# Performance work log

Hardware: AMD Instinct MI355X
Metric: run time of the kernel (lower is better)

The kernel has to match this reference:

```python
import jax, jax.numpy as jnp
import numpy as np
from jax import lax

B, A, T, D, V, K = 16, 1024, 512, 256, 50000, 3
EXP_DILS = [1, 2, 4, 8, 16, 32, 32]  # conv_num=7, exp_num=5
REF_DILS = [1, 1, 1]                 # refine_num=3


def setup_inputs() -> dict:
    key = jax.random.key(0)
    ks = jax.random.split(key, 14)
    inp = {
        'article_word': jax.random.randint(ks[0], (B, A), 0, V),
        'article_char': jax.random.randint(ks[1], (B, A, 16), 0, 100),
        'template_word': jax.random.randint(ks[2], (B, T), 0, V),
        'template_char': jax.random.randint(ks[3], (B, T, 16), 0, 100),
        'article_mask': jnp.ones((B, A), jnp.float32),
        'template_mask': jnp.ones((B, T), jnp.float32),
        'emb': jax.random.normal(ks[4], (V, D), jnp.float32) * 0.02,
        'exp_w': jax.random.normal(ks[5], (7, K, D, 2 * D), jnp.float32) * 0.03,
        'exp_b': jnp.zeros((7, 2 * D), jnp.float32),
        'ref_w': jax.random.normal(ks[6], (3, K, D, 2 * D), jnp.float32) * 0.03,
        'ref_b': jnp.zeros((3, 2 * D), jnp.float32),
        'ff1_w': jax.random.normal(ks[7], (10, 10), jnp.float32) * 0.3,
        'ff1_b': jnp.zeros((10,), jnp.float32),
        'ff2_w': jax.random.normal(ks[8], (10, 1), jnp.float32) * 0.3,
        'ff2_b': jnp.zeros((1,), jnp.float32),
    }
    return inp


def _res_block(x, w, b, dilation):
    # x: [B, L, D]; w: [K, D, 2D]  (Conv1d, padding='same' given k//2*dilation)
    pad = (K // 2) * dilation
    y = lax.conv_general_dilated(x, w, window_strides=(1,), padding=[(pad, pad)],
                                 rhs_dilation=(dilation,),
                                 dimension_numbers=('NWC', 'WIO', 'NWC')) + b
    a, g = jnp.split(y, 2, axis=2)  # GLU on channel dim
    return x + a * jax.nn.sigmoid(g)


def _encode(x, exp_w, exp_b, ref_w, ref_b):
    for i, d in enumerate(EXP_DILS):
        x = _res_block(x, exp_w[i], exp_b[i], d)
    for i, d in enumerate(REF_DILS):
        x = _res_block(x, ref_w[i], ref_b[i], d)
    return x  # dropout is identity in eval mode


def reference(article_word, article_char, template_word, template_char,
              article_mask, template_mask, emb, exp_w, exp_b, ref_w, ref_b,
              ff1_w, ff1_b, ff2_w, ff2_b):
    art = _encode(emb[article_word], exp_w, exp_b, ref_w, ref_b)    # [B,A,D]
    tpl = _encode(emb[template_word], exp_w, exp_b, ref_w, ref_b)   # [B,T,D]
    # pairwise squared distance without materializing [B,A,T,D]
    a2 = jnp.sum(art * art, axis=-1)                 # [B,A]
    t2 = jnp.sum(tpl * tpl, axis=-1)                 # [B,T]
    dot = jnp.einsum('bad,btd->bat', art, tpl)       # [B,A,T]
    dist = jnp.maximum(a2[:, :, None] + t2[:, None, :] - 2.0 * dot, 0.0)
    S = jnp.exp(-dist) * article_mask[:, :, None] * template_mask[:, None, :]
    row_max = jnp.max(S, axis=2)                     # [B,A]
    top, _ = lax.top_k(row_max, 10)                  # sorted descending, [B,10]
    h = jax.nn.relu(top @ ff1_w + ff1_b)             # [B,10]
    out = (h @ ff2_w + ff2_b).squeeze()              # [B]
    return out
```

## Files before the change

### kernel.cpp

```cpp
#include <hip/hip_runtime.h>
#include <math.h>

#define NB 16
#define NA 1024
#define NT 512
#define ND 256
#define PAD 32

typedef short bf8_t __attribute__((ext_vector_type(8)));
typedef float f4_t __attribute__((ext_vector_type(4)));

__device__ __forceinline__ float bf2f(ushort u) {
    union { unsigned int i; float f; } v; v.i = ((unsigned int)u) << 16; return v.f;
}
__device__ __forceinline__ ushort f2bf(float f) {
    union { float f; unsigned int i; } v; v.f = f;
    unsigned int x = v.i;
    unsigned int r = (x + 0x7fffu + ((x >> 16) & 1u)) >> 16;
    return (ushort)r;
}
__device__ __forceinline__ void gl_lds16(const void* g, void* l) {
    __builtin_amdgcn_global_load_lds(
        (const __attribute__((address_space(1))) unsigned int*)g,
        (__attribute__((address_space(3))) unsigned int*)l, 16, 0, 0);
}


__global__ void pad_zero(ushort* __restrict__ art_a, ushort* __restrict__ art_b,
                         ushort* __restrict__ tpl_a, ushort* __restrict__ tpl_b) {
    int y = blockIdx.y;
    ushort* p = (y == 0) ? art_a : (y == 1) ? art_b : (y == 2) ? tpl_a : tpl_b;
    int L = (y < 2) ? NA : NT;
    int Lp = L + 2 * PAD;
    int idx = blockIdx.x * 256 + threadIdx.x;
    int plane = idx >> 6;
    int row_in = idx & 63;
    int slab = (row_in < PAD) ? row_in : L + row_in;
    uint4 z = make_uint4(0, 0, 0, 0);
    *(uint4*)(p + ((size_t)plane * Lp + slab) * 8) = z;
}

__global__ void gather_emb_bf16(const int* __restrict__ words,
                                const float* __restrict__ emb,
                                ushort* __restrict__ out, int Lbits, int Lp, int n) {
    int idx = blockIdx.x * 256 + threadIdx.x;
    if (idx >= n) return;
    int L = 1 << Lbits;
    int l = idx & (L - 1);
    int bq = idx >> Lbits;
    int qq = bq & 31, b = bq >> 5;
    int wd = words[b * L + l];
    const float4* src = (const float4*)(emb + (size_t)wd * ND + qq * 8);
    float4 v0 = src[0], v1 = src[1];
    ushort o[8];
    o[0]=f2bf(v0.x); o[1]=f2bf(v0.y); o[2]=f2bf(v0.z); o[3]=f2bf(v0.w);
    o[4]=f2bf(v1.x); o[5]=f2bf(v1.y); o[6]=f2bf(v1.z); o[7]=f2bf(v1.w);
    *(uint4*)(out + ((size_t)bq * Lp + PAD + l) * 8) = *(uint4*)o;
}

__global__ void __launch_bounds__(256)
repack_w(const float* __restrict__ exp_w, const float* __restrict__ ref_w,
         ushort* __restrict__ wpack) {
    __shared__ float tile[64][65];
    int li = blockIdx.z;
    int gk = blockIdx.x;
    int gc = blockIdx.y;
    const float* src = (li < 7) ? exp_w + (size_t)li * 3 * ND * 512
                                : ref_w + (size_t)(li - 7) * 3 * ND * 512;
    int k0g = gk * 64, c0 = gc * 64;
    int tid = threadIdx.x;
    #pragma unroll
    for (int p = 0; p < 4; ++p) {
        int kr = p * 16 + (tid >> 4);
        int cc = (tid & 15) * 4;
        *(float4*)&tile[kr][cc] =
            *(const float4*)(src + (size_t)(k0g + kr) * 512 + c0 + cc);
    }
    __syncthreads();
    int tap = k0g >> 8, kl0 = k0g & 255, kc0 = kl0 >> 5;
    int ag = c0 >> 8, cb = (c0 & 255) >> 6;
    int kg = tid >> 5, idx = tid & 31;
    int kc = kc0 + (kg >> 2), qq = kg & 3;
    #pragma unroll
    for (int h = 0; h < 2; ++h) {
        int w64 = idx + h * 32;
        int cprime = h * 64 + ag * 32 + idx;
        ushort o[8];
        #pragma unroll
        for (int j = 0; j < 8; ++j) o[j] = f2bf(tile[kg * 8 + j][w64]);
        ushort* d = wpack +
            (((((size_t)(li * 4 + cb) * 3 + tap) * 8 + kc) * 4 + qq) * 128 + cprime) * 8;
        *(uint4*)d = *(uint4*)o;
    }
}

__global__ void __launch_bounds__(256, 3)
conv_glu_mfma(const ushort* __restrict__ art_x, ushort* __restrict__ art_y,
              const ushort* __restrict__ tpl_x, ushort* __restrict__ tpl_y,
              const ushort* __restrict__ wp, const float* __restrict__ bias,
              int dil) {
    __shared__ char smem[34816];
    ushort* Als = (ushort*)smem;
    float* ylds = (float*)smem;

    const int tid = threadIdx.x;
    const int w = tid >> 6, lane = tid & 63;
    const int wm = w >> 1, wn = w & 1;
    const int q = lane >> 4, l15 = lane & 15;

    const int b = blockIdx.z;
    const int plane = blockIdx.y;
    const int cb = blockIdx.x;
    const int b32 = b * 32;

    int Lp, l0;
    const ushort* xb;
    ushort* yb;
    if (plane < 8) {
        Lp = NA + 2 * PAD; l0 = plane * 128;
        xb = art_x; yb = art_y;
    } else {
        Lp = NT + 2 * PAD; l0 = (plane - 8) * 128;
        xb = tpl_x; yb = tpl_y;
    }
    const ushort* wl = wp + (size_t)cb * 98304;
    const int boff = (q * 128 + wn * 64 + l15) * 8;

    f4_t acc[4][4];
    #pragma unroll
    for (int i = 0; i < 4; ++i)
        #pragma unroll
        for (int j = 0; j < 4; ++j)
            acc[i][j] = (f4_t){0.f, 0.f, 0.f, 0.f};

    for (int kc = 0; kc < 8; ++kc) {
        bf8_t bfr[3][4];
        const ushort* wkc = wl + kc * 4096 + boff;
        #pragma unroll
        for (int t = 0; t < 3; ++t)
            #pragma unroll
            for (int nt = 0; nt < 4; ++nt)
                bfr[t][nt] = *(const bf8_t*)(wkc + t * 32768 + nt * 128);

        #pragma unroll
        for (int s3 = 0; s3 < 3; ++s3) {
            int s = w + s3 * 4;
            int qq = kc * 4 + s / 3;
            int rphys = l0 + (s % 3) * 64 + lane;
            gl_lds16(xb + ((size_t)(b32 + qq) * Lp + rphys) * 8, Als + s * 512);
        }
        __syncthreads();

        #pragma unroll
        for (int t = 0; t < 3; ++t) {
            const int sh = (t - 1) * dil;
            bf8_t af[4];
            #pragma unroll
            for (int mt = 0; mt < 4; ++mt)
                af[mt] = *(const bf8_t*)(Als + (q * 192 + 32 + sh + wm * 64 + mt * 16 + l15) * 8);
            #pragma unroll
            for (int mt = 0; mt < 4; ++mt)
                #pragma unroll
                for (int nt = 0; nt < 4; ++nt)
                    acc[mt][nt] = __builtin_amdgcn_mfma_f32_16x16x32_bf16(
                        af[mt], bfr[t][nt], acc[mt][nt], 0, 0, 0);
        }
        __syncthreads();
    }

    #pragma unroll
    for (int nt = 0; nt < 2; ++nt) {
        const int cl = wn * 32 + nt * 16 + l15;
        const int chan = cb * 64 + cl;
        const float ba = bias[chan];
        const float bg2 = bias[chan + 256];
        #pragma unroll
        for (int mt = 0; mt < 4; ++mt) {
            #pragma unroll
            for (int r = 0; r < 4; ++r) {
                const int row = wm * 64 + mt * 16 + q * 4 + r;
                float av = acc[mt][nt][r] + ba;
                float gv = acc[mt][nt + 2][r] + bg2;
                ylds[row * 68 + cl] = av / (1.f + __expf(-gv));
            }
        }
    }
    __syncthreads();

    #pragma unroll
    for (int p = 0; p < 4; ++p) {
        int u = p * 256 + tid;
        int cl8 = u >> 7;
        int row = u & 127;
        size_t go = ((size_t)(b32 + cb * 8 + cl8) * Lp + l0 + PAD + row) * 8;
        ushort xv[8]; *(uint4*)xv = *(const uint4*)(xb + go);
        float4 y0 = *(float4*)&ylds[row * 68 + cl8 * 8];
        float4 y1 = *(float4*)&ylds[row * 68 + cl8 * 8 + 4];
        ushort ov[8];
        ov[0]=f2bf(bf2f(xv[0])+y0.x); ov[1]=f2bf(bf2f(xv[1])+y0.y);
        ov[2]=f2bf(bf2f(xv[2])+y0.z); ov[3]=f2bf(bf2f(xv[3])+y0.w);
        ov[4]=f2bf(bf2f(xv[4])+y1.x); ov[5]=f2bf(bf2f(xv[5])+y1.y);
        ov[6]=f2bf(bf2f(xv[6])+y1.z); ov[7]=f2bf(bf2f(xv[7])+y1.w);
        *(uint4*)(yb + go) = *(uint4*)ov;
    }
}

__global__ void sumsq_bf16(const ushort* __restrict__ x, float* __restrict__ out,
                           int L, int Lp) {
    __shared__ float red[4][64];
    int tid = threadIdx.x;
    int r = tid & 63, pg = tid >> 6;
    int row_g = blockIdx.x * 64 + r;
    int b = row_g / L, l = row_g - b * L;
    float s = 0.f;
    #pragma unroll
    for (int j = 0; j < 8; ++j) {
        int qq = pg * 8 + j;
        const ushort* p = x + ((size_t)(b * 32 + qq) * Lp + PAD + l) * 8;
        ushort v[8]; *(uint4*)v = *(const uint4*)p;
        #pragma unroll
        for (int e = 0; e < 8; ++e) { float f = bf2f(v[e]); s += f * f; }
    }
    red[pg][r] = s;
    __syncthreads();
    if (tid < 64)
        out[blockIdx.x * 64 + tid] =
            red[0][tid] + red[1][tid] + red[2][tid] + red[3][tid];
}

__global__ void __launch_bounds__(256)
dist_rowmax_mfma(const ushort* __restrict__ art, const ushort* __restrict__ tpl,
                 const float* __restrict__ a2, const float* __restrict__ t2,
                 const float* __restrict__ amask, const float* __restrict__ tmask,
                 float* __restrict__ rmaxp) {
    __shared__ ushort Als[128 * 32];
    __shared__ ushort Bls[128 * 32];
    __shared__ float red[2][128];

    const int tid = threadIdx.x;
    const int w = tid >> 6, lane = tid & 63;
    const int wm = w >> 1, wn = w & 1;
    const int q = lane >> 4, l15 = lane & 15;

    const int b = blockIdx.y;
    const int a0 = blockIdx.x * 128;
    const int t0 = blockIdx.z * 128;
    const int b32 = b * 32;
    const int LpA = NA + 2 * PAD, LpT = NT + 2 * PAD;

    float a2v[4][4], amv[4][4];
    #pragma unroll
    for (int mt = 0; mt < 4; ++mt)
        #pragma unroll
        for (int r = 0; r < 4; ++r) {
            int row = a0 + wm * 64 + mt * 16 + q * 4 + r;
            a2v[mt][r] = a2[b * NA + row];
            amv[mt][r] = amask[b * NA + row];
        }

    f4_t acc[4][4];
    #pragma unroll
    for (int i = 0; i < 4; ++i)
        #pragma unroll
        for (int j = 0; j < 4; ++j)
            acc[i][j] = (f4_t){0.f, 0.f, 0.f, 0.f};

    for (int kb = 0; kb < 8; ++kb) {
        #pragma unroll
        for (int s3 = 0; s3 < 2; ++s3) {
            int s = w + s3 * 4;
            int qq = kb * 4 + (s >> 1);
            int r0 = (s & 1) * 64;
            gl_lds16(art + ((size_t)(b32 + qq) * LpA + PAD + a0 + r0 + lane) * 8,
                     Als + s * 512);
            gl_lds16(tpl + ((size_t)(b32 + qq) * LpT + PAD + t0 + r0 + lane) * 8,
                     Bls + s * 512);
        }
        __syncthreads();

        bf8_t af[4], bfr[4];
        #pragma unroll
        for (int mt = 0; mt < 4; ++mt)
            af[mt] = *(const bf8_t*)(Als + (q * 128 + wm * 64 + mt * 16 + l15) * 8);
        #pragma unroll
        for (int nt = 0; nt < 4; ++nt)
            bfr[nt] = *(const bf8_t*)(Bls + (q * 128 + wn * 64 + nt * 16 + l15) * 8);
        #pragma unroll
        for (int mt = 0; mt < 4; ++mt)
            #pragma unroll
            for (int nt = 0; nt < 4; ++nt)
                acc[mt][nt] = __builtin_amdgcn_mfma_f32_16x16x32_bf16(
                    af[mt], bfr[nt], acc[mt][nt], 0, 0, 0);
        __syncthreads();
    }

    float rm[4][4];
    #pragma unroll
    for (int mt = 0; mt < 4; ++mt)
        #pragma unroll
        for (int r = 0; r < 4; ++r) rm[mt][r] = 0.f;

    #pragma unroll
    for (int nt = 0; nt < 4; ++nt) {
        int t = t0 + wn * 64 + nt * 16 + l15;
        float t2v = t2[b * NT + t];
        float tmv = tmask[b * NT + t];
        #pragma unroll
        for (int mt = 0; mt < 4; ++mt)
            #pragma unroll
            for (int r = 0; r < 4; ++r) {
                float d = a2v[mt][r] + t2v - 2.f * acc[mt][nt][r];
                d = fmaxf(d, 0.f);
                float s = __expf(-d) * amv[mt][r] * tmv;
                rm[mt][r] = fmaxf(rm[mt][r], s);
            }
    }
    #pragma unroll
    for (int mt = 0; mt < 4; ++mt)
        #pragma unroll
        for (int r = 0; r < 4; ++r) {
            float v = rm[mt][r];
            #pragma unroll
            for (int off = 1; off < 16; off <<= 1)
                v = fmaxf(v, __shfl_xor(v, off));
            rm[mt][r] = v;
        }
    if (l15 == 0) {
        #pragma unroll
        for (int mt = 0; mt < 4; ++mt)
            #pragma unroll
            for (int r = 0; r < 4; ++r)
                red[wn][wm * 64 + mt * 16 + q * 4 + r] = rm[mt][r];
    }
    __syncthreads();
    if (tid < 128)
        rmaxp[((size_t)blockIdx.z * NB + b) * NA + a0 + tid] =
            fmaxf(red[0][tid], red[1][tid]);
}

__global__ void __launch_bounds__(256)
topk_mlp_kernel(const float* __restrict__ rmaxp,
                const float* __restrict__ ff1_w, const float* __restrict__ ff1_b,
                const float* __restrict__ ff2_w, const float* __restrict__ ff2_b,
                float* __restrict__ out) {
    __shared__ float vals[NA];
    __shared__ float top[10];
    __shared__ float h[10];
    __shared__ float rv[256];
    __shared__ int ri[256];

    int b = blockIdx.x;
    int tid = threadIdx.x;
    for (int i = tid; i < NA; i += 256) {
        float m = rmaxp[(size_t)b * NA + i];
        m = fmaxf(m, rmaxp[((size_t)NB + b) * NA + i]);
        m = fmaxf(m, rmaxp[((size_t)2 * NB + b) * NA + i]);
        m = fmaxf(m, rmaxp[((size_t)3 * NB + b) * NA + i]);
        vals[i] = m;
    }
    __syncthreads();

    for (int it = 0; it < 10; ++it) {
        float best = -1e30f;
        int bi = 0;
        for (int i = tid; i < NA; i += 256) {
            if (vals[i] > best) { best = vals[i]; bi = i; }
        }
        rv[tid] = best; ri[tid] = bi;
        __syncthreads();
        for (int s = 128; s; s >>= 1) {
            if (tid < s) {
                if (rv[tid + s] > rv[tid]) { rv[tid] = rv[tid + s]; ri[tid] = ri[tid + s]; }
            }
            __syncthreads();
        }
        if (tid == 0) { top[it] = rv[0]; vals[ri[0]] = -1e30f; }
        __syncthreads();
    }

    if (tid < 10) {
        float s = ff1_b[tid];
        #pragma unroll
        for (int i = 0; i < 10; ++i) s += top[i] * ff1_w[i * 10 + tid];
        h[tid] = fmaxf(s, 0.f);
    }
    __syncthreads();
    if (tid == 0) {
        float s = ff2_b[0];
        #pragma unroll
        for (int j = 0; j < 10; ++j) s += h[j] * ff2_w[j];
        out[b] = s;
    }
}

extern "C" void kernel_launch(void* const* d_in, const int* in_sizes, int n_in,
                              void* d_out, int out_size, void* d_ws, size_t ws_size,
                              hipStream_t stream) {
    const int*   art_w = (const int*)d_in[0];
    const int*   tpl_w = (const int*)d_in[2];
    const float* amask = (const float*)d_in[4];
    const float* tmask = (const float*)d_in[5];
    const float* emb   = (const float*)d_in[6];
    const float* exp_w = (const float*)d_in[7];
    const float* exp_b = (const float*)d_in[8];
    const float* ref_w = (const float*)d_in[9];
    const float* ref_b = (const float*)d_in[10];
    const float* ff1_w = (const float*)d_in[11];
    const float* ff1_b = (const float*)d_in[12];
    const float* ff2_w = (const float*)d_in[13];
    const float* ff2_b = (const float*)d_in[14];
    float* out = (float*)d_out;

    const size_t art_bytes = (size_t)NB * 32 * (NA + 2 * PAD) * 8 * 2;
    const size_t tpl_bytes = (size_t)NB * 32 * (NT + 2 * PAD) * 8 * 2;
    const size_t wpk_bytes = (size_t)10 * 4 * 3 * 8 * 4 * 128 * 8 * 2;

    char* p = (char*)d_ws;
    ushort* art_a = (ushort*)p; p += art_bytes;
    ushort* art_b = (ushort*)p; p += art_bytes;
    ushort* tpl_a = (ushort*)p; p += tpl_bytes;
    ushort* tpl_b = (ushort*)p; p += tpl_bytes;
    ushort* wpack = (ushort*)p; p += wpk_bytes;
    float* a2    = (float*)p; p += (size_t)NB * NA * 4;
    float* t2    = (float*)p; p += (size_t)NB * NT * 4;
    float* rmaxp = (float*)p; p += (size_t)4 * NB * NA * 4;

    pad_zero<<<dim3(128, 4), 256, 0, stream>>>(art_a, art_b, tpl_a, tpl_b);
    repack_w<<<dim3(12, 8, 10), 256, 0, stream>>>(exp_w, ref_w, wpack);

    {
        int n = NB * 32 * NA;
        gather_emb_bf16<<<(n + 255) / 256, 256, 0, stream>>>(art_w, emb, art_a, 10, NA + 64, n);
        n = NB * 32 * NT;
        gather_emb_bf16<<<(n + 255) / 256, 256, 0, stream>>>(tpl_w, emb, tpl_a, 9, NT + 64, n);
    }

    const int dils[10] = {1, 2, 4, 8, 16, 32, 32, 1, 1, 1};

    ushort* a_cur = art_a; ushort* a_nxt = art_b;
    ushort* t_cur = tpl_a; ushort* t_nxt = tpl_b;
    for (int i = 0; i < 10; ++i) {
        const ushort* wl = wpack + (size_t)i * 4 * 98304;
        const float* bb = (i < 7) ? exp_b + (size_t)i * 512
                                  : ref_b + (size_t)(i - 7) * 512;
        conv_glu_mfma<<<dim3(4, 12, NB), 256, 0, stream>>>(
            a_cur, a_nxt, t_cur, t_nxt, wl, bb, dils[i]);
        ushort* t1 = a_cur; a_cur = a_nxt; a_nxt = t1;
        ushort* t2p = t_cur; t_cur = t_nxt; t_nxt = t2p;
    }
    ushort* art_fin = a_cur;
    ushort* tpl_fin = t_cur;

    sumsq_bf16<<<(NB * NA) / 64, 256, 0, stream>>>(art_fin, a2, NA, NA + 64);
    sumsq_bf16<<<(NB * NT) / 64, 256, 0, stream>>>(tpl_fin, t2, NT, NT + 64);

    dist_rowmax_mfma<<<dim3(NA / 128, NB, 4), 256, 0, stream>>>(
        art_fin, tpl_fin, a2, t2, amask, tmask, rmaxp);

    topk_mlp_kernel<<<NB, 256, 0, stream>>>(rmaxp, ff1_w, ff1_b, ff2_w, ff2_b, out);
}
```

Baseline: 422.1 us.

## Remap block ids for XCD locality, double K-chunk staging, shuffle-based top-k

```diff
diff --git a/kernel.cpp b/kernel.cpp
--- a/kernel.cpp
+++ b/kernel.cpp
@@ -108,9 +108,11 @@
     const int wm = w >> 1, wn = w & 1;
     const int q = lane >> 4, l15 = lane & 15;
 
-    const int b = blockIdx.z;
-    const int plane = blockIdx.y;
-    const int cb = blockIdx.x;
+    const int id = blockIdx.x;
+    const int cb = (id >> 3) & 3;
+    const int pb = ((id >> 5) << 3) | (id & 7);
+    const int plane = pb % 12;
+    const int b = pb / 12;
     const int b32 = b * 32;
 
     int Lp, l0;
@@ -133,37 +135,43 @@
         for (int j = 0; j < 4; ++j)
             acc[i][j] = (f4_t){0.f, 0.f, 0.f, 0.f};
 
-    for (int kc = 0; kc < 8; ++kc) {
-        bf8_t bfr[3][4];
-        const ushort* wkc = wl + kc * 4096 + boff;
-        #pragma unroll
-        for (int t = 0; t < 3; ++t)
-            #pragma unroll
-            for (int nt = 0; nt < 4; ++nt)
-                bfr[t][nt] = *(const bf8_t*)(wkc + t * 32768 + nt * 128);
-
-        #pragma unroll
-        for (int s3 = 0; s3 < 3; ++s3) {
+    for (int kc2 = 0; kc2 < 4; ++kc2) {
+        #pragma unroll
+        for (int s3 = 0; s3 < 6; ++s3) {
             int s = w + s3 * 4;
-            int qq = kc * 4 + s / 3;
-            int rphys = l0 + (s % 3) * 64 + lane;
+            int h = s / 12, within = s % 12;
+            int qq = kc2 * 8 + h * 4 + within / 3;
+            int rphys = l0 + (within % 3) * 64 + lane;
             gl_lds16(xb + ((size_t)(b32 + qq) * Lp + rphys) * 8, Als + s * 512);
         }
         __syncthreads();
 
         #pragma unroll
-        for (int t = 0; t < 3; ++t) {
-            const int sh = (t - 1) * dil;
-            bf8_t af[4];
-            #pragma unroll
-            for (int mt = 0; mt < 4; ++mt)
-                af[mt] = *(const bf8_t*)(Als + (q * 192 + 32 + sh + wm * 64 + mt * 16 + l15) * 8);
-            #pragma unroll
-            for (int mt = 0; mt < 4; ++mt)
+        for (int h = 0; h < 2; ++h) {
+            const int kc = kc2 * 2 + h;
+            bf8_t bfr[3][4];
+            const ushort* wkc = wl + kc * 4096 + boff;
+            #pragma unroll
+            for (int t = 0; t < 3; ++t)
                 #pragma unroll
                 for (int nt = 0; nt < 4; ++nt)
-                    acc[mt][nt] = __builtin_amdgcn_mfma_f32_16x16x32_bf16(
-                        af[mt], bfr[t][nt], acc[mt][nt], 0, 0, 0);
+                    bfr[t][nt] = *(const bf8_t*)(wkc + t * 32768 + nt * 128);
+
+            const ushort* Ah = Als + h * 6144;
+            #pragma unroll
+            for (int t = 0; t < 3; ++t) {
+                const int sh = (t - 1) * dil;
+                bf8_t af[4];
+                #pragma unroll
+                for (int mt = 0; mt < 4; ++mt)
+                    af[mt] = *(const bf8_t*)(Ah + (q * 192 + 32 + sh + wm * 64 + mt * 16 + l15) * 8);
+                #pragma unroll
+                for (int mt = 0; mt < 4; ++mt)
+                    #pragma unroll
+                    for (int nt = 0; nt < 4; ++nt)
+                        acc[mt][nt] = __builtin_amdgcn_mfma_f32_16x16x32_bf16(
+                            af[mt], bfr[t][nt], acc[mt][nt], 0, 0, 0);
+            }
         }
         __syncthreads();
     }
@@ -242,9 +250,12 @@
     const int wm = w >> 1, wn = w & 1;
     const int q = lane >> 4, l15 = lane & 15;
 
-    const int b = blockIdx.y;
-    const int a0 = blockIdx.x * 128;
-    const int t0 = blockIdx.z * 128;
+    const int id = blockIdx.x;
+    const int b = (id & 7) | (((id >> 3) & 1) << 3);
+    const int rest = id >> 4;
+    const int a0 = (rest & 7) * 128;
+    const int tplane = rest >> 3;
+    const int t0 = tplane * 128;
     const int b32 = b * 32;
     const int LpA = NA + 2 * PAD, LpT = NT + 2 * PAD;
 
@@ -334,7 +345,7 @@
     }
     __syncthreads();
     if (tid < 128)
-        rmaxp[((size_t)blockIdx.z * NB + b) * NA + a0 + tid] =
+        rmaxp[((size_t)tplane * NB + b) * NA + a0 + tid] =
             fmaxf(red[0][tid], red[1][tid]);
 }
 
@@ -346,11 +357,12 @@
     __shared__ float vals[NA];
     __shared__ float top[10];
     __shared__ float h[10];
-    __shared__ float rv[256];
-    __shared__ int ri[256];
+    __shared__ float rv[4];
+    __shared__ int ri[4];
 
     int b = blockIdx.x;
     int tid = threadIdx.x;
+    int lane = tid & 63, wv = tid >> 6;
     for (int i = tid; i < NA; i += 256) {
         float m = rmaxp[(size_t)b * NA + i];
         m = fmaxf(m, rmaxp[((size_t)NB + b) * NA + i]);
@@ -363,18 +375,26 @@
     for (int it = 0; it < 10; ++it) {
         float best = -1e30f;
         int bi = 0;
-        for (int i = tid; i < NA; i += 256) {
+        #pragma unroll
+        for (int u = 0; u < 4; ++u) {
+            int i = u * 256 + tid;
             if (vals[i] > best) { best = vals[i]; bi = i; }
         }
-        rv[tid] = best; ri[tid] = bi;
-        __syncthreads();
-        for (int s = 128; s; s >>= 1) {
-            if (tid < s) {
-                if (rv[tid + s] > rv[tid]) { rv[tid] = rv[tid + s]; ri[tid] = ri[tid + s]; }
-            }
-            __syncthreads();
-        }
-        if (tid == 0) { top[it] = rv[0]; vals[ri[0]] = -1e30f; }
+        #pragma unroll
+        for (int off = 32; off; off >>= 1) {
+            float ob = __shfl_down(best, off);
+            int oi = __shfl_down(bi, off);
+            if (ob > best) { best = ob; bi = oi; }
+        }
+        if (lane == 0) { rv[wv] = best; ri[wv] = bi; }
+        __syncthreads();
+        if (tid == 0) {
+            float bb = rv[0]; int bbi = ri[0];
+            #pragma unroll
+            for (int k = 1; k < 4; ++k)
+                if (rv[k] > bb) { bb = rv[k]; bbi = ri[k]; }
+            top[it] = bb; vals[bbi] = -1e30f;
+        }
         __syncthreads();
     }
 
@@ -443,7 +463,7 @@
         const ushort* wl = wpack + (size_t)i * 4 * 98304;
         const float* bb = (i < 7) ? exp_b + (size_t)i * 512
                                   : ref_b + (size_t)(i - 7) * 512;
-        conv_glu_mfma<<<dim3(4, 12, NB), 256, 0, stream>>>(
+        conv_glu_mfma<<<768, 256, 0, stream>>>(
             a_cur, a_nxt, t_cur, t_nxt, wl, bb, dils[i]);
         ushort* t1 = a_cur; a_cur = a_nxt; a_nxt = t1;
         ushort* t2p = t_cur; t_cur = t_nxt; t_nxt = t2p;
@@ -454,7 +474,7 @@
     sumsq_bf16<<<(NB * NA) / 64, 256, 0, stream>>>(art_fin, a2, NA, NA + 64);
     sumsq_bf16<<<(NB * NT) / 64, 256, 0, stream>>>(tpl_fin, t2, NT, NT + 64);
 
-    dist_rowmax_mfma<<<dim3(NA / 128, NB, 4), 256, 0, stream>>>(
+    dist_rowmax_mfma<<<512, 256, 0, stream>>>(
         art_fin, tpl_fin, a2, t2, amask, tmask, rmaxp);
 
     topk_mlp_kernel<<<NB, 256, 0, stream>>>(rmaxp, ff1_w, ff1_b, ff2_w, ff2_b, out);
```

After: 387.0 us. 8.3% less time.
